# Kernel tuning notes

Measured on AMD Instinct MI355X. Metric: run time of the kernel, lower is better.

## Reference

```python
import jax, jax.numpy as jnp
import numpy as np

EMBED_DIM = 1024
NUM_HEADS = 16
HEAD_DIM = EMBED_DIM // NUM_HEADS
STD = 0.02


def setup_inputs() -> dict:
    key = jax.random.key(0)
    k1, k2, k3 = jax.random.split(key, 3)
    B, S = 2, 2048
    inputs = jax.random.normal(k1, (B, S, EMBED_DIM), dtype=jnp.float32)
    # qkv projection: Linear(E, 3E); torch Linear weight is [out, in]
    w_qkv = jax.random.normal(k2, (3 * EMBED_DIM, EMBED_DIM), dtype=jnp.float32) * STD
    b_qkv = jnp.zeros((3 * EMBED_DIM,), dtype=jnp.float32)
    w_out = jax.random.normal(k3, (EMBED_DIM, EMBED_DIM), dtype=jnp.float32) * STD
    b_out = jnp.zeros((EMBED_DIM,), dtype=jnp.float32)
    return {"inputs": inputs, "w_qkv": w_qkv, "b_qkv": b_qkv, "w_out": w_out, "b_out": b_out}


def reference(inputs, w_qkv, b_qkv, w_out, b_out):
    B, S, E = inputs.shape
    qkv = inputs @ w_qkv.T + b_qkv                      # [B,S,3E]
    q, k, v = jnp.split(qkv, 3, axis=2)                 # each [B,S,E]

    def split_heads(t):
        return t.reshape(B, S, NUM_HEADS, HEAD_DIM).transpose(0, 2, 1, 3)  # [B,H,S,D]

    q, k, v = split_heads(q), split_heads(k), split_heads(v)
    scores = jnp.einsum('bhqd,bhkd->bhqk', q, k) * (1.0 / np.sqrt(HEAD_DIM))
    causal = jnp.tril(jnp.ones((S, S), dtype=bool))     # [S,S]
    scores = jnp.where(causal[None, None, :, :], scores, -jnp.inf)
    probs = jax.nn.softmax(scores, axis=-1)             # dropout is identity in eval mode
    ctx = jnp.einsum('bhqk,bhkd->bhqd', probs, v)       # [B,H,S,D]
    ctx = ctx.transpose(0, 2, 1, 3).reshape(B, S, E)
    return ctx @ w_out.T + b_out
```

## Files before the change

kernel.cpp:

```cpp
#include <hip/hip_runtime.h>
#include <hip/hip_bf16.h>

#define BATCH 2
#define SEQ   2048
#define EMB   1024
#define NHEAD 16
#define HDIM  64
#define MTOT  (BATCH*SEQ)
#define KTOT  EMB

#define NX  (MTOT*EMB)
#define NW1 (3*EMB*EMB)
#define NW2 (EMB*EMB)

typedef short bf8 __attribute__((ext_vector_type(8)));
typedef short s4v __attribute__((ext_vector_type(4)));
typedef float f4  __attribute__((ext_vector_type(4)));
typedef unsigned int uint;

__device__ __forceinline__ short f2b(float f) {
    __hip_bfloat16 h = __float2bfloat16(f);
    return __builtin_bit_cast(short, h);
}
__device__ __forceinline__ void gl_lds16(const short* g, short* l) {
    __builtin_amdgcn_global_load_lds(
        (const __attribute__((address_space(1))) uint*)g,
        (__attribute__((address_space(3))) uint*)l, 16, 0, 0);
}
#define SWZ_SRC(lane)      ((((lane) ^ ((lane)>>2) ^ ((lane)>>4)) & 3) * 8)
#define SWZ_RD(quad, l16)  ((((quad) ^ (l16) ^ ((l16)>>2)) & 3) * 8)

__global__ __launch_bounds__(256) void cvt_all(
    const float* __restrict__ X, const float* __restrict__ W1,
    const float* __restrict__ W2,
    short* __restrict__ xb, short* __restrict__ w1b, short* __restrict__ w2b)
{
    int i4 = (blockIdx.x * 256 + threadIdx.x) * 4;
    const float* src; short* dst; int off;
    if (i4 < NX)            { src = X;  dst = xb;  off = i4; }
    else if (i4 < NX + NW1) { src = W1; dst = w1b; off = i4 - NX; }
    else                    { src = W2; dst = w2b; off = i4 - NX - NW1; }
    float4 v = *(const float4*)&src[off];
    s4v o; o[0]=f2b(v.x); o[1]=f2b(v.y); o[2]=f2b(v.z); o[3]=f2b(v.w);
    *(s4v*)&dst[off] = o;
}

__global__ __launch_bounds__(256) void gemm_qkv(
    const short* __restrict__ Xb, const short* __restrict__ Wb,
    const float* __restrict__ bias,
    short* __restrict__ qb, short* __restrict__ kb, short* __restrict__ vtb)
{
    __shared__ __align__(16) short As[2][128*32];
    __shared__ __align__(16) short Bs[2][128*32];
    const int tid  = threadIdx.x;
    const int lane = tid & 63;
    const int w    = tid >> 6;
    const int l16  = lane & 15, quad = lane >> 4;
    const int wm   = (w >> 1) * 64, wn = (w & 1) * 64;
    const int srow = (lane >> 2);
    const int scol = SWZ_SRC(lane);
    f4 acc[4][4] = {};

    auto stage = [&](int k0, int b) {
        #pragma unroll
        for (int t = 0; t < 2; t++) {
            int ra = blockIdx.x*128 + w*32 + t*16 + srow;
            gl_lds16(&Xb[(size_t)ra*KTOT + k0 + scol], &As[b][(w*32 + t*16)*32]);
            int rb = blockIdx.y*128 + w*32 + t*16 + srow;
            gl_lds16(&Wb[(size_t)rb*KTOT + k0 + scol], &Bs[b][(w*32 + t*16)*32]);
        }
    };

    stage(0, 0);
    __syncthreads();
    int buf = 0;
    for (int k0 = 0; k0 < KTOT; k0 += 32) {
        if (k0 + 32 < KTOT) stage(k0 + 32, buf ^ 1);
        bf8 af[4], bf[4];
        #pragma unroll
        for (int i = 0; i < 4; i++) {
            af[i] = *(const bf8*)&As[buf][(wm + i*16 + l16)*32 + SWZ_RD(quad, l16)];
            bf[i] = *(const bf8*)&Bs[buf][(wn + i*16 + l16)*32 + SWZ_RD(quad, l16)];
        }
        #pragma unroll
        for (int mt = 0; mt < 4; mt++)
            #pragma unroll
            for (int nt = 0; nt < 4; nt++)
                acc[mt][nt] = __builtin_amdgcn_mfma_f32_16x16x32_bf16(af[mt], bf[nt], acc[mt][nt], 0, 0, 0);
        __syncthreads();
        buf ^= 1;
    }
    #pragma unroll
    for (int mt = 0; mt < 4; mt++)
    #pragma unroll
    for (int nt = 0; nt < 4; nt++) {
        int colg = blockIdx.y*128 + wn + nt*16 + l16;
        float bv = bias[colg];
        #pragma unroll
        for (int r = 0; r < 4; r++) {
            int rowg = blockIdx.x*128 + wm + mt*16 + quad*4 + r;
            short h = f2b(acc[mt][nt][r] + bv);
            int bb = rowg >> 11, s = rowg & 2047;
            if (colg < 1024) {
                int hh = colg >> 6, d = colg & 63;
                qb[(((bb*NHEAD + hh)*SEQ + s) << 6) + d] = h;
            } else if (colg < 2048) {
                int c2 = colg - 1024, hh = c2 >> 6, d = c2 & 63;
                kb[(((bb*NHEAD + hh)*SEQ + s) << 6) + d] = h;
            } else {
                int c3 = colg - 2048, hh = c3 >> 6, d = c3 & 63;
                int ssw = (s & ~63) | (((s & 15) << 2) | ((s >> 4) & 3));
                vtb[((bb*NHEAD + hh)*HDIM + d)*SEQ + ssw] = h;
            }
        }
    }
}

__global__ __launch_bounds__(256, 4) void attn(
    const short* __restrict__ qb, const short* __restrict__ kb,
    const short* __restrict__ vtb, short* __restrict__ ctx)
{
    __shared__ __align__(16) short Ks[2*2*64*32];
    __shared__ __align__(16) short Vs[2*2*64*32];
    __shared__ __align__(16) short pl[4][16*64];
    const int tid = threadIdx.x;
    const int w = tid >> 6, lane = tid & 63;
    const int l16 = lane & 15, quad = lane >> 4;
    const int f  = blockIdx.x;
    const int bh = ((f & 7) << 2) + ((f >> 3) & 3);
    const int tq = 31 - (f >> 5);
    const int q0w = tq*64 + w*16;
    const int base = bh * (SEQ*HDIM);
    short* myp = pl[w];
    const float SC = 0.125f * 1.44269504f;

    const int lq  = lane >> 2;
    const int lsw = SWZ_SRC(lane);

    bf8 qa[2];
    #pragma unroll
    for (int kc = 0; kc < 2; kc++)
        qa[kc] = *(const bf8*)&qb[base + (q0w + l16)*HDIM + kc*32 + quad*8];

    f4 o[4] = {};
    float lacc[4] = {};
    const int lastj = q0w + 15;
    const int jmax  = tq*64 + 64;

    auto dma_stage = [&](int j0, int b) {
        #pragma unroll
        for (int tt = 0; tt < 4; tt++) {
            const int t = w*4 + tt;
            const int cc = t & 1, g = (t >> 1) & 3;
            if (t < 8) {
                gl_lds16(&kb[base + (j0 + g*16 + lq)*HDIM + cc*32 + lsw],
                         &Ks[b*4096 + (cc*64 + g*16)*32]);
            } else {
                gl_lds16(&vtb[base + (g*16 + lq)*SEQ + j0 + cc*32 + lsw],
                         &Vs[b*4096 + (cc*64 + g*16)*32]);
            }
        }
    };

    dma_stage(0, 0);
    __syncthreads();
    int buf = 0;
    for (int j0 = 0; j0 < jmax; j0 += 64) {
        if (j0 + 64 < jmax) dma_stage(j0 + 64, buf ^ 1);
        if (j0 <= lastj) {
            f4 s[4] = {};
            #pragma unroll
            for (int kf = 0; kf < 4; kf++)
                #pragma unroll
                for (int c = 0; c < 2; c++) {
                    bf8 kfr = *(const bf8*)&Ks[buf*4096 + (c*64 + kf*16 + l16)*32 + SWZ_RD(quad, l16)];
                    s[kf] = __builtin_amdgcn_mfma_f32_16x16x32_bf16(qa[c], kfr, s[kf], 0, 0, 0);
                }
            const bool needmask = (j0 + 63 > q0w);
            #pragma unroll
            for (int r = 0; r < 4; r++) {
                const int row = quad*4 + r;
                const int qi  = q0w + row;
                float e[4];
                #pragma unroll
                for (int kf = 0; kf < 4; kf++) {
                    e[kf] = __builtin_amdgcn_exp2f(s[kf][r] * SC);
                    if (needmask && (j0 + kf*16 + l16 > qi)) e[kf] = 0.0f;
                    lacc[r] += e[kf];
                }
                uint u01 = __builtin_amdgcn_perm(__builtin_bit_cast(uint, e[1]),
                                                 __builtin_bit_cast(uint, e[0]), 0x07060302u);
                uint u23 = __builtin_amdgcn_perm(__builtin_bit_cast(uint, e[3]),
                                                 __builtin_bit_cast(uint, e[2]), 0x07060302u);
                uint2 pk = {u01, u23};
                int c8 = ((l16 >> 1) ^ (row & 7));
                *(uint2*)&myp[row*64 + c8*8 + (l16 & 1)*4] = pk;
            }
            asm volatile("" ::: "memory");
            bf8 pa[2];
            #pragma unroll
            for (int kc = 0; kc < 2; kc++)
                pa[kc] = *(const bf8*)&myp[l16*64 + (((kc*4 + quad) ^ (l16 & 7)))*8];
            #pragma unroll
            for (int dt = 0; dt < 4; dt++)
                #pragma unroll
                for (int c = 0; c < 2; c++) {
                    bf8 vf = *(const bf8*)&Vs[buf*4096 + (c*64 + dt*16 + l16)*32 + SWZ_RD(quad, l16)];
                    o[dt] = __builtin_amdgcn_mfma_f32_16x16x32_bf16(pa[c], vf, o[dt], 0, 0, 0);
                }
        }
        __syncthreads();
        buf ^= 1;
    }
    #pragma unroll
    for (int r = 0; r < 4; r++) {
        float v = lacc[r];
        v += __shfl_xor(v, 1);
        v += __shfl_xor(v, 2);
        v += __shfl_xor(v, 4);
        v += __shfl_xor(v, 8);
        lacc[r] = v;
    }
    const int b = bh >> 4, h = bh & 15;
    #pragma unroll
    for (int r = 0; r < 4; r++) {
        float inv = 1.0f / lacc[r];
        int qi = q0w + quad*4 + r;
        int rowoff = (b*SEQ + qi)*EMB + h*HDIM;
        #pragma unroll
        for (int dt = 0; dt < 4; dt++)
            ctx[rowoff + dt*16 + l16] = f2b(o[dt][r] * inv);
    }
}

__global__ __launch_bounds__(256) void gemm_out(
    const short* __restrict__ A, const short* __restrict__ Wb,
    const float* __restrict__ bias, float* __restrict__ out)
{
    __shared__ __align__(16) short As[2][2*128*32];
    __shared__ __align__(16) short Bs[2][2*128*32];
    const int tid  = threadIdx.x;
    const int lane = tid & 63;
    const int w    = tid >> 6;
    const int l16  = lane & 15, quad = lane >> 4;
    const int wm   = (w >> 1) * 64, wn = (w & 1) * 64;
    const int srow = (lane >> 2);
    const int scol = SWZ_SRC(lane);
    f4 acc[4][4] = {};

    auto stage = [&](int k0, int b) {
        #pragma unroll
        for (int t = 0; t < 4; t++) {
            const int rr = w*32 + (t & 1)*16;
            const int kc = t >> 1;
            int ra = blockIdx.x*128 + rr + srow;
            gl_lds16(&A[(size_t)ra*KTOT + k0 + kc*32 + scol],  &As[b][kc*4096 + rr*32]);
            int rb = blockIdx.y*128 + rr + srow;
            gl_lds16(&Wb[(size_t)rb*KTOT + k0 + kc*32 + scol], &Bs[b][kc*4096 + rr*32]);
        }
    };

    stage(0, 0);
    __syncthreads();
    int buf = 0;
    for (int k0 = 0; k0 < KTOT; k0 += 64) {
        if (k0 + 64 < KTOT) stage(k0 + 64, buf ^ 1);
        #pragma unroll
        for (int kc = 0; kc < 2; kc++) {
            bf8 af[4], bf[4];
            #pragma unroll
            for (int i = 0; i < 4; i++) {
                af[i] = *(const bf8*)&As[buf][kc*4096 + (wm + i*16 + l16)*32 + SWZ_RD(quad, l16)];
                bf[i] = *(const bf8*)&Bs[buf][kc*4096 + (wn + i*16 + l16)*32 + SWZ_RD(quad, l16)];
            }
            #pragma unroll
            for (int mt = 0; mt < 4; mt++)
                #pragma unroll
                for (int nt = 0; nt < 4; nt++)
                    acc[mt][nt] = __builtin_amdgcn_mfma_f32_16x16x32_bf16(af[mt], bf[nt], acc[mt][nt], 0, 0, 0);
        }
        __syncthreads();
        buf ^= 1;
    }
    #pragma unroll
    for (int mt = 0; mt < 4; mt++)
    #pragma unroll
    for (int nt = 0; nt < 4; nt++) {
        int colg = blockIdx.y*128 + wn + nt*16 + l16;
        float bv = bias[colg];
        #pragma unroll
        for (int r = 0; r < 4; r++) {
            int rowg = blockIdx.x*128 + wm + mt*16 + quad*4 + r;
            out[(size_t)rowg*EMB + colg] = acc[mt][nt][r] + bv;
        }
    }
}

extern "C" void kernel_launch(void* const* d_in, const int* in_sizes, int n_in,
                              void* d_out, int out_size, void* d_ws, size_t ws_size,
                              hipStream_t stream) {
    const float* X    = (const float*)d_in[0];
    const float* Wqkv = (const float*)d_in[1];
    const float* Bqkv = (const float*)d_in[2];
    const float* Wout = (const float*)d_in[3];
    const float* Bout = (const float*)d_in[4];
    float* out = (float*)d_out;

    short* xb    = (short*)d_ws;
    short* w1b   = xb  + NX;
    short* w2b   = w1b + NW1;
    short* qb    = w2b + NW2;
    short* kb    = qb  + NX;
    short* vtb   = kb  + NX;
    short* ctx   = vtb + NX;

    cvt_all<<<(NX+NW1+NW2)/1024, 256, 0, stream>>>(X, Wqkv, Wout, xb, w1b, w2b);
    dim3 g1(MTOT/128, 3*EMB/128);
    gemm_qkv<<<g1, 256, 0, stream>>>(xb, w1b, Bqkv, qb, kb, vtb);
    attn<<<dim3(1024), 256, 0, stream>>>(qb, kb, vtb, ctx);
    dim3 g3(MTOT/128, EMB/128);
    gemm_out<<<g3, 256, 0, stream>>>(ctx, w2b, Bout, out);
}
```

Baseline: 186.9 us.

## Remap GEMM blocks per XCD, shrink out-GEMM tiles, restructure attention loop

Both GEMMs now use a 1D grid remapped so that blocks sharing weight columns land on the same XCD, which should improve L2 reuse. Both drop LDS double buffering in favour of a single buffer synchronised on each k-step. The output GEMM tile is cut from 128x128 to 64x64, giving 1024 blocks for more occupancy and parallelism. The attention kernel reorders query tiles to balance causal work across CUs and splits K/V loads by wave using precomputed pointers. It also limits masking to the diagonal tile and drops the loop bound checks. Losing double buffering risks exposing global load latency.

```diff
diff --git a/kernel.cpp b/kernel.cpp
--- a/kernel.cpp
+++ b/kernel.cpp
@@ -50,8 +50,12 @@
     const float* __restrict__ bias,
     short* __restrict__ qb, short* __restrict__ kb, short* __restrict__ vtb)
 {
-    __shared__ __align__(16) short As[2][128*32];
-    __shared__ __align__(16) short Bs[2][128*32];
+    __shared__ __align__(16) short As[128*32];
+    __shared__ __align__(16) short Bs[128*32];
+    const int f = blockIdx.x;
+    const int xcd = f & 7, i = f >> 3;
+    const int by = xcd*3 + (i % 3);
+    const int bx = i / 3;
     const int tid  = threadIdx.x;
     const int lane = tid & 63;
     const int w    = tid >> 6;
@@ -60,27 +64,20 @@
     const int srow = (lane >> 2);
     const int scol = SWZ_SRC(lane);
     f4 acc[4][4] = {};
-
-    auto stage = [&](int k0, int b) {
+    for (int k0 = 0; k0 < KTOT; k0 += 32) {
         #pragma unroll
         for (int t = 0; t < 2; t++) {
-            int ra = blockIdx.x*128 + w*32 + t*16 + srow;
-            gl_lds16(&Xb[(size_t)ra*KTOT + k0 + scol], &As[b][(w*32 + t*16)*32]);
-            int rb = blockIdx.y*128 + w*32 + t*16 + srow;
-            gl_lds16(&Wb[(size_t)rb*KTOT + k0 + scol], &Bs[b][(w*32 + t*16)*32]);
-        }
-    };
-
-    stage(0, 0);
-    __syncthreads();
-    int buf = 0;
-    for (int k0 = 0; k0 < KTOT; k0 += 32) {
-        if (k0 + 32 < KTOT) stage(k0 + 32, buf ^ 1);
+            int ra = bx*128 + w*32 + t*16 + srow;
+            gl_lds16(&Xb[(size_t)ra*KTOT + k0 + scol], &As[(w*32 + t*16)*32]);
+            int rb = by*128 + w*32 + t*16 + srow;
+            gl_lds16(&Wb[(size_t)rb*KTOT + k0 + scol], &Bs[(w*32 + t*16)*32]);
+        }
+        __syncthreads();
         bf8 af[4], bf[4];
         #pragma unroll
-        for (int i = 0; i < 4; i++) {
-            af[i] = *(const bf8*)&As[buf][(wm + i*16 + l16)*32 + SWZ_RD(quad, l16)];
-            bf[i] = *(const bf8*)&Bs[buf][(wn + i*16 + l16)*32 + SWZ_RD(quad, l16)];
+        for (int t = 0; t < 4; t++) {
+            af[t] = *(const bf8*)&As[(wm + t*16 + l16)*32 + SWZ_RD(quad, l16)];
+            bf[t] = *(const bf8*)&Bs[(wn + t*16 + l16)*32 + SWZ_RD(quad, l16)];
         }
         #pragma unroll
         for (int mt = 0; mt < 4; mt++)
@@ -88,17 +85,16 @@
             for (int nt = 0; nt < 4; nt++)
                 acc[mt][nt] = __builtin_amdgcn_mfma_f32_16x16x32_bf16(af[mt], bf[nt], acc[mt][nt], 0, 0, 0);
         __syncthreads();
-        buf ^= 1;
     }
     #pragma unroll
     for (int mt = 0; mt < 4; mt++)
     #pragma unroll
     for (int nt = 0; nt < 4; nt++) {
-        int colg = blockIdx.y*128 + wn + nt*16 + l16;
+        int colg = by*128 + wn + nt*16 + l16;
         float bv = bias[colg];
         #pragma unroll
         for (int r = 0; r < 4; r++) {
-            int rowg = blockIdx.x*128 + wm + mt*16 + quad*4 + r;
+            int rowg = bx*128 + wm + mt*16 + quad*4 + r;
             short h = f2b(acc[mt][nt][r] + bv);
             int bb = rowg >> 11, s = rowg & 2047;
             if (colg < 1024) {
@@ -120,15 +116,18 @@
     const short* __restrict__ qb, const short* __restrict__ kb,
     const short* __restrict__ vtb, short* __restrict__ ctx)
 {
-    __shared__ __align__(16) short Ks[2*2*64*32];
-    __shared__ __align__(16) short Vs[2*2*64*32];
+    __shared__ __align__(16) short Ks[2*4096];
+    __shared__ __align__(16) short Vs[2*4096];
     __shared__ __align__(16) short pl[4][16*64];
     const int tid = threadIdx.x;
     const int w = tid >> 6, lane = tid & 63;
     const int l16 = lane & 15, quad = lane >> 4;
     const int f  = blockIdx.x;
-    const int bh = ((f & 7) << 2) + ((f >> 3) & 3);
-    const int tq = 31 - (f >> 5);
+    const int bh = f & 31;
+    const int j5 = (f >> 5) & 7;
+    const int hq = f >> 8;
+    const int tq = (hq == 0) ? j5 : (hq == 1) ? (15 - j5)
+                 : (hq == 2) ? (16 + j5) : (31 - j5);
     const int q0w = tq*64 + w*16;
     const int base = bh * (SEQ*HDIM);
     short* myp = pl[w];
@@ -137,6 +136,24 @@
     const int lq  = lane >> 2;
     const int lsw = SWZ_SRC(lane);
 
+    const bool isk = (w < 2);
+    short* tb = isk ? Ks : Vs;
+    const int sstep = isk ? 64*HDIM : 64;
+    const short* sp0; const short* sp1; const short* sp2; const short* sp3;
+    int dof[4];
+    {
+        const int wb2 = (w & 1) * 4;
+        #pragma unroll
+        for (int tt = 0; tt < 4; tt++) {
+            int t = wb2 + tt, cc = t & 1, g = (t >> 1) & 3;
+            dof[tt] = (cc*64 + g*16)*32;
+            const short* s = isk ? &kb[base + (g*16 + lq)*HDIM + cc*32 + lsw]
+                                 : &vtb[base + (g*16 + lq)*SEQ + cc*32 + lsw];
+            if (tt == 0) sp0 = s; else if (tt == 1) sp1 = s;
+            else if (tt == 2) sp2 = s; else sp3 = s;
+        }
+    }
+
     bf8 qa[2];
     #pragma unroll
     for (int kc = 0; kc < 2; kc++)
@@ -144,39 +161,32 @@
 
     f4 o[4] = {};
     float lacc[4] = {};
-    const int lastj = q0w + 15;
-    const int jmax  = tq*64 + 64;
-
-    auto dma_stage = [&](int j0, int b) {
-        #pragma unroll
-        for (int tt = 0; tt < 4; tt++) {
-            const int t = w*4 + tt;
-            const int cc = t & 1, g = (t >> 1) & 3;
-            if (t < 8) {
-                gl_lds16(&kb[base + (j0 + g*16 + lq)*HDIM + cc*32 + lsw],
-                         &Ks[b*4096 + (cc*64 + g*16)*32]);
-            } else {
-                gl_lds16(&vtb[base + (g*16 + lq)*SEQ + j0 + cc*32 + lsw],
-                         &Vs[b*4096 + (cc*64 + g*16)*32]);
-            }
-        }
-    };
-
-    dma_stage(0, 0);
+    const int rdK = l16*32 + SWZ_RD(quad, l16);
+
+    gl_lds16(sp0, tb + dof[0]); gl_lds16(sp1, tb + dof[1]);
+    gl_lds16(sp2, tb + dof[2]); gl_lds16(sp3, tb + dof[3]);
+    sp0 += sstep; sp1 += sstep; sp2 += sstep; sp3 += sstep;
     __syncthreads();
+
     int buf = 0;
-    for (int j0 = 0; j0 < jmax; j0 += 64) {
-        if (j0 + 64 < jmax) dma_stage(j0 + 64, buf ^ 1);
-        if (j0 <= lastj) {
-            f4 s[4] = {};
-            #pragma unroll
-            for (int kf = 0; kf < 4; kf++)
-                #pragma unroll
-                for (int c = 0; c < 2; c++) {
-                    bf8 kfr = *(const bf8*)&Ks[buf*4096 + (c*64 + kf*16 + l16)*32 + SWZ_RD(quad, l16)];
-                    s[kf] = __builtin_amdgcn_mfma_f32_16x16x32_bf16(qa[c], kfr, s[kf], 0, 0, 0);
-                }
-            const bool needmask = (j0 + 63 > q0w);
+    for (int st = 0; st <= tq; st++) {
+        if (st < tq) {
+            short* d = tb + (buf ^ 1)*4096;
+            gl_lds16(sp0, d + dof[0]); gl_lds16(sp1, d + dof[1]);
+            gl_lds16(sp2, d + dof[2]); gl_lds16(sp3, d + dof[3]);
+            sp0 += sstep; sp1 += sstep; sp2 += sstep; sp3 += sstep;
+        }
+        const int kbase = buf*4096 + rdK;
+        f4 s[4] = {};
+        #pragma unroll
+        for (int kf = 0; kf < 4; kf++)
+            #pragma unroll
+            for (int c = 0; c < 2; c++) {
+                bf8 kfr = *(const bf8*)&Ks[kbase + (c*64 + kf*16)*32];
+                s[kf] = __builtin_amdgcn_mfma_f32_16x16x32_bf16(qa[c], kfr, s[kf], 0, 0, 0);
+            }
+        if (st == tq) {
+            const int j0 = st*64;
             #pragma unroll
             for (int r = 0; r < 4; r++) {
                 const int row = quad*4 + r;
@@ -185,7 +195,7 @@
                 #pragma unroll
                 for (int kf = 0; kf < 4; kf++) {
                     e[kf] = __builtin_amdgcn_exp2f(s[kf][r] * SC);
-                    if (needmask && (j0 + kf*16 + l16 > qi)) e[kf] = 0.0f;
+                    if (j0 + kf*16 + l16 > qi) e[kf] = 0.0f;
                     lacc[r] += e[kf];
                 }
                 uint u01 = __builtin_amdgcn_perm(__builtin_bit_cast(uint, e[1]),
@@ -196,19 +206,37 @@
                 int c8 = ((l16 >> 1) ^ (row & 7));
                 *(uint2*)&myp[row*64 + c8*8 + (l16 & 1)*4] = pk;
             }
-            asm volatile("" ::: "memory");
-            bf8 pa[2];
-            #pragma unroll
-            for (int kc = 0; kc < 2; kc++)
-                pa[kc] = *(const bf8*)&myp[l16*64 + (((kc*4 + quad) ^ (l16 & 7)))*8];
-            #pragma unroll
-            for (int dt = 0; dt < 4; dt++)
+        } else {
+            #pragma unroll
+            for (int r = 0; r < 4; r++) {
+                const int row = quad*4 + r;
+                float e[4];
                 #pragma unroll
-                for (int c = 0; c < 2; c++) {
-                    bf8 vf = *(const bf8*)&Vs[buf*4096 + (c*64 + dt*16 + l16)*32 + SWZ_RD(quad, l16)];
-                    o[dt] = __builtin_amdgcn_mfma_f32_16x16x32_bf16(pa[c], vf, o[dt], 0, 0, 0);
+                for (int kf = 0; kf < 4; kf++) {
+                    e[kf] = __builtin_amdgcn_exp2f(s[kf][r] * SC);
+                    lacc[r] += e[kf];
                 }
-        }
+                uint u01 = __builtin_amdgcn_perm(__builtin_bit_cast(uint, e[1]),
+                                                 __builtin_bit_cast(uint, e[0]), 0x07060302u);
+                uint u23 = __builtin_amdgcn_perm(__builtin_bit_cast(uint, e[3]),
+                                                 __builtin_bit_cast(uint, e[2]), 0x07060302u);
+                uint2 pk = {u01, u23};
+                int c8 = ((l16 >> 1) ^ (row & 7));
+                *(uint2*)&myp[row*64 + c8*8 + (l16 & 1)*4] = pk;
+            }
+        }
+        asm volatile("" ::: "memory");
+        bf8 pa[2];
+        #pragma unroll
+        for (int kc = 0; kc < 2; kc++)
+            pa[kc] = *(const bf8*)&myp[l16*64 + (((kc*4 + quad) ^ (l16 & 7)))*8];
+        #pragma unroll
+        for (int dt = 0; dt < 4; dt++)
+            #pragma unroll
+            for (int c = 0; c < 2; c++) {
+                bf8 vf = *(const bf8*)&Vs[kbase + (c*64 + dt*16)*32];
+                o[dt] = __builtin_amdgcn_mfma_f32_16x16x32_bf16(pa[c], vf, o[dt], 0, 0, 0);
+            }
         __syncthreads();
         buf ^= 1;
     }
@@ -237,60 +265,50 @@
     const short* __restrict__ A, const short* __restrict__ Wb,
     const float* __restrict__ bias, float* __restrict__ out)
 {
-    __shared__ __align__(16) short As[2][2*128*32];
-    __shared__ __align__(16) short Bs[2][2*128*32];
+    __shared__ __align__(16) short As[64*32];
+    __shared__ __align__(16) short Bs[64*32];
+    const int f = blockIdx.x;
+    const int xcd = f & 7, i = f >> 3;
+    const int by = xcd*2 + (i & 1);
+    const int bx = i >> 1;
     const int tid  = threadIdx.x;
     const int lane = tid & 63;
     const int w    = tid >> 6;
     const int l16  = lane & 15, quad = lane >> 4;
-    const int wm   = (w >> 1) * 64, wn = (w & 1) * 64;
+    const int wm   = (w >> 1) * 32, wn = (w & 1) * 32;
     const int srow = (lane >> 2);
     const int scol = SWZ_SRC(lane);
-    f4 acc[4][4] = {};
-
-    auto stage = [&](int k0, int b) {
-        #pragma unroll
-        for (int t = 0; t < 4; t++) {
-            const int rr = w*32 + (t & 1)*16;
-            const int kc = t >> 1;
-            int ra = blockIdx.x*128 + rr + srow;
-            gl_lds16(&A[(size_t)ra*KTOT + k0 + kc*32 + scol],  &As[b][kc*4096 + rr*32]);
-            int rb = blockIdx.y*128 + rr + srow;
-            gl_lds16(&Wb[(size_t)rb*KTOT + k0 + kc*32 + scol], &Bs[b][kc*4096 + rr*32]);
-        }
-    };
-
-    stage(0, 0);
-    __syncthreads();
-    int buf = 0;
-    for (int k0 = 0; k0 < KTOT; k0 += 64) {
-        if (k0 + 64 < KTOT) stage(k0 + 64, buf ^ 1);
-        #pragma unroll
-        for (int kc = 0; kc < 2; kc++) {
-            bf8 af[4], bf[4];
-            #pragma unroll
-            for (int i = 0; i < 4; i++) {
-                af[i] = *(const bf8*)&As[buf][kc*4096 + (wm + i*16 + l16)*32 + SWZ_RD(quad, l16)];
-                bf[i] = *(const bf8*)&Bs[buf][kc*4096 + (wn + i*16 + l16)*32 + SWZ_RD(quad, l16)];
-            }
-            #pragma unroll
-            for (int mt = 0; mt < 4; mt++)
-                #pragma unroll
-                for (int nt = 0; nt < 4; nt++)
-                    acc[mt][nt] = __builtin_amdgcn_mfma_f32_16x16x32_bf16(af[mt], bf[nt], acc[mt][nt], 0, 0, 0);
-        }
-        __syncthreads();
-        buf ^= 1;
-    }
-    #pragma unroll
-    for (int mt = 0; mt < 4; mt++)
-    #pragma unroll
-    for (int nt = 0; nt < 4; nt++) {
-        int colg = blockIdx.y*128 + wn + nt*16 + l16;
+    f4 acc[2][2] = {};
+    for (int k0 = 0; k0 < KTOT; k0 += 32) {
+        {
+            int ra = bx*64 + w*16 + srow;
+            gl_lds16(&A[(size_t)ra*KTOT + k0 + scol],  &As[(w*16)*32]);
+            int rb = by*64 + w*16 + srow;
+            gl_lds16(&Wb[(size_t)rb*KTOT + k0 + scol], &Bs[(w*16)*32]);
+        }
+        __syncthreads();
+        bf8 af[2], bf[2];
+        #pragma unroll
+        for (int t = 0; t < 2; t++) {
+            af[t] = *(const bf8*)&As[(wm + t*16 + l16)*32 + SWZ_RD(quad, l16)];
+            bf[t] = *(const bf8*)&Bs[(wn + t*16 + l16)*32 + SWZ_RD(quad, l16)];
+        }
+        #pragma unroll
+        for (int mt = 0; mt < 2; mt++)
+            #pragma unroll
+            for (int nt = 0; nt < 2; nt++)
+                acc[mt][nt] = __builtin_amdgcn_mfma_f32_16x16x32_bf16(af[mt], bf[nt], acc[mt][nt], 0, 0, 0);
+        __syncthreads();
+    }
+    #pragma unroll
+    for (int mt = 0; mt < 2; mt++)
+    #pragma unroll
+    for (int nt = 0; nt < 2; nt++) {
+        int colg = by*64 + wn + nt*16 + l16;
         float bv = bias[colg];
         #pragma unroll
         for (int r = 0; r < 4; r++) {
-            int rowg = blockIdx.x*128 + wm + mt*16 + quad*4 + r;
+            int rowg = bx*64 + wm + mt*16 + quad*4 + r;
             out[(size_t)rowg*EMB + colg] = acc[mt][nt][r] + bv;
         }
     }
@@ -315,9 +333,7 @@
     short* ctx   = vtb + NX;
 
     cvt_all<<<(NX+NW1+NW2)/1024, 256, 0, stream>>>(X, Wqkv, Wout, xb, w1b, w2b);
-    dim3 g1(MTOT/128, 3*EMB/128);
-    gemm_qkv<<<g1, 256, 0, stream>>>(xb, w1b, Bqkv, qb, kb, vtb);
+    gemm_qkv<<<dim3(768), 256, 0, stream>>>(xb, w1b, Bqkv, qb, kb, vtb);
     attn<<<dim3(1024), 256, 0, stream>>>(qb, kb, vtb, ctx);
-    dim3 g3(MTOT/128, EMB/128);
-    gemm_out<<<g3, 256, 0, stream>>>(ctx, w2b, Bout, out);
-}
+    gemm_out<<<dim3(1024), 256, 0, stream>>>(ctx, w2b, Bout, out);
+}
```

Result: slower. 193.5 us (+3.5%).
